# Optimization experiments

Measured on AMD Instinct MI355X. Metric: run time of the kernel, lower is better.

Reference implementation:

```python
import jax, jax.numpy as jnp
import numpy as np

D_IN = 300      # mol2vec feature dim
H = 64          # neurons[0] == neurons[1]


def _l2norm(x):
    # F.normalize(x, p=2, dim=-1)
    n = jnp.sqrt(jnp.sum(x * x, axis=-1, keepdims=True))
    return x / jnp.maximum(n, 1e-12)


def _scatter_mean(x, row, col, n_nodes):
    # scatter_mean(x[col], row, dim_size=n_nodes); empty rows -> 0
    s = jax.ops.segment_sum(x[col], row, num_segments=n_nodes)
    c = jax.ops.segment_sum(jnp.ones((row.shape[0], 1), x.dtype), row, num_segments=n_nodes)
    return s / jnp.maximum(c, 1.0)


def _sage_base(x, edges, W, b, n_nodes):
    agg = _scatter_mean(x, edges[0], edges[1], n_nodes)
    h = jnp.concatenate([agg, x], axis=1) @ W + b
    return _l2norm(h)


def _sage_deep(x1, x2, pos_e, neg_e, W, b, n_nodes):
    a1 = _scatter_mean(x1, pos_e[0], pos_e[1], n_nodes)
    a2 = _scatter_mean(x2, neg_e[0], neg_e[1], n_nodes)
    h = jnp.concatenate([a1, a2, x1], axis=1) @ W + b
    return _l2norm(h)


def setup_inputs() -> dict:
    key = jax.random.key(0)
    ks = jax.random.split(key, 16)
    N, E = 8192, 262144

    X = jax.random.normal(ks[0], (N, D_IN), dtype=jnp.float32)

    def make_edges(k):
        e = jax.random.randint(k, (2, E), 0, N, dtype=jnp.int64)
        # no self loops (module calls remove_self_loops)
        col = jnp.where(e[1] == e[0], (e[1] + 1) % N, e[1])
        return jnp.stack([e[0], col])

    positive_edges = make_edges(ks[1])
    negative_edges = make_edges(ks[2])

    labels = jax.random.normal(ks[3], (N * N,), dtype=jnp.float32)
    label_mask = jax.random.uniform(ks[4], (N, N), dtype=jnp.float32)

    sd = lambda fan_in: 1.0 / np.sqrt(fan_in)
    W_pos_base = jax.random.normal(ks[5], (2 * D_IN, H), dtype=jnp.float32) * sd(2 * D_IN)
    b_pos_base = jnp.zeros((H,), dtype=jnp.float32)
    W_neg_base = jax.random.normal(ks[6], (2 * D_IN, H), dtype=jnp.float32) * sd(2 * D_IN)
    b_neg_base = jnp.zeros((H,), dtype=jnp.float32)
    W_pos_deep = jax.random.normal(ks[7], (3 * H, H), dtype=jnp.float32) * sd(3 * H)
    b_pos_deep = jnp.zeros((H,), dtype=jnp.float32)
    W_neg_deep = jax.random.normal(ks[8], (3 * H, H), dtype=jnp.float32) * sd(3 * H)
    b_neg_deep = jnp.zeros((H,), dtype=jnp.float32)

    return {
        "X": X, "positive_edges": positive_edges, "negative_edges": negative_edges,
        "labels": labels, "label_mask": label_mask,
        "W_pos_base": W_pos_base, "b_pos_base": b_pos_base,
        "W_neg_base": W_neg_base, "b_neg_base": b_neg_base,
        "W_pos_deep": W_pos_deep, "b_pos_deep": b_pos_deep,
        "W_neg_deep": W_neg_deep, "b_neg_deep": b_neg_deep,
    }


def reference(X, positive_edges, negative_edges, labels, label_mask,
              W_pos_base, b_pos_base, W_neg_base, b_neg_base,
              W_pos_deep, b_pos_deep, W_neg_deep, b_neg_deep):
    N = X.shape[0]
    h_pos = jnp.tanh(_sage_base(X, positive_edges, W_pos_base, b_pos_base, N))
    h_neg = jnp.tanh(_sage_base(X, negative_edges, W_neg_base, b_neg_base, N))
    h_pos2 = jnp.tanh(_sage_deep(h_pos, h_neg, positive_edges, negative_edges, W_pos_deep, b_pos_deep, N))
    h_neg2 = jnp.tanh(_sage_deep(h_neg, h_pos, positive_edges, negative_edges, W_neg_deep, b_neg_deep, N))
    z = jnp.concatenate([h_pos2, h_neg2], axis=1)           # [N, 2H]
    X_mol = _l2norm(z)
    pred = ((X_mol @ X_mol.T) * label_mask).reshape(-1)      # [N*N]
    loss = jnp.mean((pred - labels) ** 2)
    return (loss, X_mol, pred)
```

## Files before the change

### kernel.cpp

```cpp
#include <hip/hip_runtime.h>
#include <hip/hip_bf16.h>

#define DIN 300
#define KP  320
#define NH  64

typedef __bf16 bf16x8 __attribute__((ext_vector_type(8)));
typedef float  f32x4  __attribute__((ext_vector_type(4)));

__device__ inline float wave_sum(float v){
#pragma unroll
  for (int m = 32; m >= 1; m >>= 1) v += __shfl_xor(v, m, 64);
  return v;
}

__global__ __launch_bounds__(256) void k_cvtX(const float* __restrict__ X,
                                              __hip_bfloat16* __restrict__ Xb){
  int row = blockIdx.x;
  const float* xr = X + (size_t)row * DIN;
  __hip_bfloat16* o = Xb + (size_t)row * KP;
  for (int k = threadIdx.x; k < KP; k += 256)
    o[k] = __float2bfloat16(k < DIN ? xr[k] : 0.f);
}

__global__ __launch_bounds__(256) void k_cvtW(const float* __restrict__ Wpb,
                                              const float* __restrict__ Wnb,
                                              __hip_bfloat16* __restrict__ Wtb){
  int c = blockIdx.x;
  int sel = c >> 6, jj = c & 63;
  const float* W = (sel < 2 ? Wpb : Wnb) + (size_t)(sel & 1) * DIN * NH + jj;
  __hip_bfloat16* o = Wtb + (size_t)c * KP;
  for (int k = threadIdx.x; k < KP; k += 256)
    o[k] = __float2bfloat16(k < DIN ? W[(size_t)k * NH] : 0.f);
}

__global__ __launch_bounds__(256) void k_gemm_base(const __hip_bfloat16* __restrict__ Xb,
                                                   const __hip_bfloat16* __restrict__ Wtb,
                                                   float* __restrict__ XW){
  const int wave = threadIdx.x >> 6, lane = threadIdx.x & 63;
  const int ti = blockIdx.y * 64 + wave * 16;
  const int cj = blockIdx.x * 64;
  const int r0 = lane & 15, kq = (lane >> 4) * 8;
  const unsigned short* Xp = (const unsigned short*)Xb;
  const unsigned short* Wp = (const unsigned short*)Wtb;
  f32x4 acc[4] = {};
  for (int ks = 0; ks < KP / 32; ++ks){
    int kb = ks * 32 + kq;
    bf16x8 a = *(const bf16x8*)(Xp + (size_t)(ti + r0) * KP + kb);
#pragma unroll
    for (int js = 0; js < 4; ++js){
      bf16x8 b = *(const bf16x8*)(Wp + (size_t)(cj + js * 16 + r0) * KP + kb);
      acc[js] = __builtin_amdgcn_mfma_f32_16x16x32_bf16(a, b, acc[js], 0, 0, 0);
    }
  }
  const int orow = ti + (lane >> 4) * 4;
  const int oc = cj + (lane & 15);
#pragma unroll
  for (int js = 0; js < 4; ++js)
#pragma unroll
    for (int i = 0; i < 4; ++i)
      XW[(size_t)(orow + i) * 256 + oc + js * 16] = acc[js][i];
}

__global__ void k_hist(const int* __restrict__ pr, const int* __restrict__ nr,
                       int* __restrict__ cp, int* __restrict__ cn, int E){
  int i = blockIdx.x * 256 + threadIdx.x;
  if (i < E){ atomicAdd(cp + pr[i], 1); atomicAdd(cn + nr[i], 1); }
}

__global__ __launch_bounds__(1024) void k_scan(const int* __restrict__ c0, int* __restrict__ o0,
                                               const int* __restrict__ c1, int* __restrict__ o1, int n){
  const int* cnt = blockIdx.x ? c1 : c0;
  int* off = blockIdx.x ? o1 : o0;
  __shared__ int lds[1024];
  int t = threadIdx.x;
  int ept = n >> 10;
  int s = 0;
  for (int i = 0; i < ept; ++i) s += cnt[t * ept + i];
  lds[t] = s; __syncthreads();
  for (int d = 1; d < 1024; d <<= 1){
    int add = (t >= d) ? lds[t - d] : 0;
    __syncthreads();
    lds[t] += add;
    __syncthreads();
  }
  int base = t ? lds[t - 1] : 0;
  for (int i = 0; i < ept; ++i){ off[t * ept + i] = base; base += cnt[t * ept + i]; }
}

__global__ void k_fill(const int* __restrict__ pr, const int* __restrict__ pc,
                       const int* __restrict__ nr, const int* __restrict__ nc,
                       const int* __restrict__ op, const int* __restrict__ on,
                       int* __restrict__ curp, int* __restrict__ curn,
                       int* __restrict__ adjp, int* __restrict__ adjn, int E){
  int i = blockIdx.x * 256 + threadIdx.x;
  if (i < E){
    int r = pr[i]; int p = atomicAdd(curp + r, 1); adjp[op[r] + p] = pc[i];
    r = nr[i];     p = atomicAdd(curn + r, 1);     adjn[on[r] + p] = nc[i];
  }
}

__device__ inline float gather_mean(const float* __restrict__ XW, const int* __restrict__ adj,
                                    int base, int d, int col){
  float s = 0.f; int j = 0;
  for (; j + 4 <= d; j += 4){
    int n0 = adj[base + j], n1 = adj[base + j + 1], n2 = adj[base + j + 2], n3 = adj[base + j + 3];
    s += XW[(size_t)n0 * 256 + col] + XW[(size_t)n1 * 256 + col]
       + XW[(size_t)n2 * 256 + col] + XW[(size_t)n3 * 256 + col];
  }
  for (; j < d; ++j) s += XW[(size_t)adj[base + j] * 256 + col];
  return s / (float)(d > 0 ? d : 1);
}

__global__ __launch_bounds__(256) void k_base(const float* __restrict__ XW,
    const int* __restrict__ adjp, const int* __restrict__ offp, const int* __restrict__ cntp,
    const int* __restrict__ adjn, const int* __restrict__ offn, const int* __restrict__ cntn,
    const float* __restrict__ bp, const float* __restrict__ bn,
    float* __restrict__ hp, float* __restrict__ hn){
  const int wave = threadIdx.x >> 6, lane = threadIdx.x & 63;
  const int node = blockIdx.x * 4 + wave;
  {
    float s = gather_mean(XW, adjp, offp[node], cntp[node], lane);
    float pre = s + XW[(size_t)node * 256 + 64 + lane] + bp[lane];
    float nrm = sqrtf(wave_sum(pre * pre));
    hp[(size_t)node * 64 + lane] = tanhf(pre / fmaxf(nrm, 1e-12f));
  }
  {
    float s = gather_mean(XW, adjn, offn[node], cntn[node], lane + 128);
    float pre = s + XW[(size_t)node * 256 + 192 + lane] + bn[lane];
    float nrm = sqrtf(wave_sum(pre * pre));
    hn[(size_t)node * 64 + lane] = tanhf(pre / fmaxf(nrm, 1e-12f));
  }
}

__global__ __launch_bounds__(256) void k_deep(const float* __restrict__ hp, const float* __restrict__ hn,
    const int* __restrict__ adjp, const int* __restrict__ offp, const int* __restrict__ cntp,
    const int* __restrict__ adjn, const int* __restrict__ offn, const int* __restrict__ cntn,
    const float* __restrict__ Wpd, const float* __restrict__ bpd,
    const float* __restrict__ Wnd, const float* __restrict__ bnd,
    float* __restrict__ xmol, __hip_bfloat16* __restrict__ Xmb){
  const int wave = threadIdx.x >> 6, lane = threadIdx.x & 63;
  const int node = blockIdx.x * 4 + wave;
  const float mhp = hp[(size_t)node * 64 + lane];
  const float mhn = hn[(size_t)node * 64 + lane];
  float a1p = 0.f, a1n = 0.f;
  {
    int d = cntp[node], base = offp[node]; int j = 0;
    for (; j + 2 <= d; j += 2){
      int n0 = adjp[base + j], n1 = adjp[base + j + 1];
      a1p += hp[(size_t)n0 * 64 + lane] + hp[(size_t)n1 * 64 + lane];
      a1n += hn[(size_t)n0 * 64 + lane] + hn[(size_t)n1 * 64 + lane];
    }
    for (; j < d; ++j){ int n0 = adjp[base + j]; a1p += hp[(size_t)n0 * 64 + lane]; a1n += hn[(size_t)n0 * 64 + lane]; }
    float inv = 1.f / (float)(d > 0 ? d : 1); a1p *= inv; a1n *= inv;
  }
  float a2p = 0.f, a2n = 0.f;
  {
    int d = cntn[node], base = offn[node]; int j = 0;
    for (; j + 2 <= d; j += 2){
      int n0 = adjn[base + j], n1 = adjn[base + j + 1];
      a2p += hn[(size_t)n0 * 64 + lane] + hn[(size_t)n1 * 64 + lane];
      a2n += hp[(size_t)n0 * 64 + lane] + hp[(size_t)n1 * 64 + lane];
    }
    for (; j < d; ++j){ int n0 = adjn[base + j]; a2p += hn[(size_t)n0 * 64 + lane]; a2n += hp[(size_t)n0 * 64 + lane]; }
    float inv = 1.f / (float)(d > 0 ? d : 1); a2p *= inv; a2n *= inv;
  }
  float accp = bpd[lane], accn = bnd[lane];
#pragma unroll 4
  for (int k = 0; k < 64; ++k){
    float p1 = __shfl(a1p, k, 64), p2 = __shfl(a2p, k, 64), p3 = __shfl(mhp, k, 64);
    float q1 = __shfl(a1n, k, 64), q2 = __shfl(a2n, k, 64), q3 = __shfl(mhn, k, 64);
    accp += p1 * Wpd[k * 64 + lane] + p2 * Wpd[(64 + k) * 64 + lane] + p3 * Wpd[(128 + k) * 64 + lane];
    accn += q1 * Wnd[k * 64 + lane] + q2 * Wnd[(64 + k) * 64 + lane] + q3 * Wnd[(128 + k) * 64 + lane];
  }
  float np = sqrtf(wave_sum(accp * accp));
  float h2p = tanhf(accp / fmaxf(np, 1e-12f));
  float nn = sqrtf(wave_sum(accn * accn));
  float h2n = tanhf(accn / fmaxf(nn, 1e-12f));
  float nz = sqrtf(wave_sum(h2p * h2p + h2n * h2n));
  float xp = h2p / fmaxf(nz, 1e-12f);
  float xn = h2n / fmaxf(nz, 1e-12f);
  xmol[(size_t)node * 128 + lane] = xp;
  xmol[(size_t)node * 128 + 64 + lane] = xn;
  Xmb[(size_t)node * 128 + lane] = __float2bfloat16(xp);
  Xmb[(size_t)node * 128 + 64 + lane] = __float2bfloat16(xn);
}

__global__ __launch_bounds__(256) void k_pred(const __hip_bfloat16* __restrict__ Xmb,
    const float* __restrict__ mask, const float* __restrict__ labels,
    float* __restrict__ pred, float* __restrict__ partial, int N){
  const int wave = threadIdx.x >> 6, lane = threadIdx.x & 63;
  const int ti = blockIdx.y * 64 + wave * 16;
  const int tj = blockIdx.x * 128;
  const int r0 = lane & 15, kq = (lane >> 4) * 8;
  const unsigned short* X = (const unsigned short*)Xmb;
  f32x4 acc[2][4] = {};
#pragma unroll
  for (int ks = 0; ks < 4; ++ks){
    int kb = ks * 32 + kq;
    bf16x8 a = *(const bf16x8*)(X + (size_t)(ti + r0) * 128 + kb);
#pragma unroll
    for (int pan = 0; pan < 2; ++pan)
#pragma unroll
      for (int js = 0; js < 4; ++js){
        bf16x8 b = *(const bf16x8*)(X + (size_t)(tj + pan * 64 + js * 16 + r0) * 128 + kb);
        acc[pan][js] = __builtin_amdgcn_mfma_f32_16x16x32_bf16(a, b, acc[pan][js], 0, 0, 0);
      }
  }
  __shared__ float tile[4][16][132];
  __shared__ float wsum[4];
  const int rb = (lane >> 4) * 4, c16 = lane & 15;
#pragma unroll
  for (int pan = 0; pan < 2; ++pan)
#pragma unroll
    for (int js = 0; js < 4; ++js)
#pragma unroll
      for (int i = 0; i < 4; ++i)
        tile[wave][rb + i][pan * 64 + js * 16 + c16] = acc[pan][js][i];
  const int hi = lane >> 5, c = lane & 31;
  f32x4 m[8], lb[8];
#pragma unroll
  for (int g = 0; g < 8; ++g){
    size_t idx = (size_t)(ti + g * 2 + hi) * N + tj + c * 4;
    m[g]  = __builtin_nontemporal_load((const f32x4*)(mask + idx));
    lb[g] = __builtin_nontemporal_load((const f32x4*)(labels + idx));
  }
  float lsum = 0.f;
#pragma unroll
  for (int g = 0; g < 8; ++g){
    int row = g * 2 + hi;
    f32x4 a = *(const f32x4*)&tile[wave][row][c * 4];
    f32x4 pv = a * m[g];
    f32x4 d = pv - lb[g];
    lsum += d[0]*d[0] + d[1]*d[1] + d[2]*d[2] + d[3]*d[3];
    size_t idx = (size_t)(ti + row) * N + tj + c * 4;
    __builtin_nontemporal_store(pv[0], pred + idx);
    __builtin_nontemporal_store(pv[1], pred + idx + 1);
    __builtin_nontemporal_store(pv[2], pred + idx + 2);
    __builtin_nontemporal_store(pv[3], pred + idx + 3);
  }
  lsum = wave_sum(lsum);
  if (lane == 0) wsum[wave] = lsum;
  __syncthreads();
  if (threadIdx.x == 0)
    partial[blockIdx.y * gridDim.x + blockIdx.x] = wsum[0] + wsum[1] + wsum[2] + wsum[3];
}

__global__ __launch_bounds__(1024) void k_loss_fin(const float* __restrict__ partial,
                                                   float* __restrict__ out, float inv, int n){
  float s = 0.f;
  for (int i = threadIdx.x; i < n; i += 1024) s += partial[i];
  s = wave_sum(s);
  __shared__ float ws[16];
  if ((threadIdx.x & 63) == 0) ws[threadIdx.x >> 6] = s;
  __syncthreads();
  if (threadIdx.x == 0){
    float t = 0.f;
#pragma unroll
    for (int w = 0; w < 16; ++w) t += ws[w];
    out[0] = t * inv;
  }
}

extern "C" void kernel_launch(void* const* d_in, const int* in_sizes, int n_in,
                              void* d_out, int out_size, void* d_ws, size_t ws_size,
                              hipStream_t stream){
  const float* X      = (const float*)d_in[0];
  const int*   pe     = (const int*)d_in[1];
  const int*   ne     = (const int*)d_in[2];
  const float* labels = (const float*)d_in[3];
  const float* mask   = (const float*)d_in[4];
  const float* Wpb    = (const float*)d_in[5];
  const float* bpb    = (const float*)d_in[6];
  const float* Wnb    = (const float*)d_in[7];
  const float* bnb    = (const float*)d_in[8];
  const float* Wpd    = (const float*)d_in[9];
  const float* bpd    = (const float*)d_in[10];
  const float* Wnd    = (const float*)d_in[11];
  const float* bnd    = (const float*)d_in[12];
  const int N = in_sizes[0] / DIN;
  const int E = in_sizes[1] / 2;

  char* ws = (char*)d_ws;
  size_t off = 0;
  auto alloc = [&](size_t bytes){ void* p = ws + off; off = (off + bytes + 255) & ~(size_t)255; return p; };
  float* XW            = (float*)alloc((size_t)N * 256 * 4);
  float* hp            = (float*)alloc((size_t)N * 64 * 4);
  float* hn            = (float*)alloc((size_t)N * 64 * 4);
  __hip_bfloat16* Xmb  = (__hip_bfloat16*)alloc((size_t)N * 128 * 2);
  __hip_bfloat16* Xb   = (__hip_bfloat16*)alloc((size_t)N * KP * 2);
  __hip_bfloat16* Wtb  = (__hip_bfloat16*)alloc((size_t)256 * KP * 2);
  int* adjp            = (int*)alloc((size_t)E * 4);
  int* adjn            = (int*)alloc((size_t)E * 4);
  char* zbase = ws + off;
  int* cntp            = (int*)alloc((size_t)N * 4);
  int* cntn            = (int*)alloc((size_t)N * 4);
  int* curp            = (int*)alloc((size_t)N * 4);
  int* curn            = (int*)alloc((size_t)N * 4);
  size_t zbytes = (size_t)((ws + off) - zbase);
  int* offp            = (int*)alloc((size_t)N * 4);
  int* offn            = (int*)alloc((size_t)N * 4);
  float* partial       = (float*)alloc((size_t)(N / 64) * (N / 128) * 4);
  (void)ws_size; (void)n_in; (void)out_size;

  float* out_loss = (float*)d_out;
  float* out_xmol = out_loss + 1;
  float* out_pred = out_xmol + (size_t)N * 128;

  hipMemsetAsync(zbase, 0, zbytes, stream);
  k_cvtX<<<N, 256, 0, stream>>>(X, Xb);
  k_cvtW<<<256, 256, 0, stream>>>(Wpb, Wnb, Wtb);
  k_gemm_base<<<dim3(4, N / 64), 256, 0, stream>>>(Xb, Wtb, XW);
  k_hist<<<(E + 255) / 256, 256, 0, stream>>>(pe, ne, cntp, cntn, E);
  k_scan<<<2, 1024, 0, stream>>>(cntp, offp, cntn, offn, N);
  k_fill<<<(E + 255) / 256, 256, 0, stream>>>(pe, pe + E, ne, ne + E, offp, offn, curp, curn, adjp, adjn, E);
  k_base<<<N / 4, 256, 0, stream>>>(XW, adjp, offp, cntp, adjn, offn, cntn, bpb, bnb, hp, hn);
  k_deep<<<N / 4, 256, 0, stream>>>(hp, hn, adjp, offp, cntp, adjn, offn, cntn,
                                    Wpd, bpd, Wnd, bnd, out_xmol, Xmb);
  k_pred<<<dim3(N / 128, N / 64), 256, 0, stream>>>(Xmb, mask, labels, out_pred, partial, N);
  k_loss_fin<<<1, 1024, 0, stream>>>(partial, out_loss, 1.0f / ((float)N * (float)N), (N / 64) * (N / 128));
}
```

Before: 365.3 us.

## Make k_pred persistent over column chunks with double-buffered mask/label loads

Each k_pred block now walks a 2048-column chunk in 16 tiles of 128 columns instead of handling one tile. The A fragment stays in registers across tiles, and mask/label loads for the next tile are issued before the current tile is consumed, using two register buffers and sched barriers. This aims to overlap the memory-bound mask/label streaming with MFMA work and cut block launch overhead. The cost is higher register pressure (launch bounds now ask for 2 blocks per SIMD) and far fewer blocks, which may reduce latency hiding.

```diff
diff --git a/kernel.cpp b/kernel.cpp
--- a/kernel.cpp
+++ b/kernel.cpp
@@ -4,6 +4,8 @@
 #define DIN 300
 #define KP  320
 #define NH  64
+#define CHUNK 2048
+#define NT (CHUNK / 128)
 
 typedef __bf16 bf16x8 __attribute__((ext_vector_type(8)));
 typedef float  f32x4  __attribute__((ext_vector_type(4)));
@@ -186,59 +188,88 @@
   Xmb[(size_t)node * 128 + 64 + lane] = __float2bfloat16(xn);
 }
 
-__global__ __launch_bounds__(256) void k_pred(const __hip_bfloat16* __restrict__ Xmb,
+__global__ __launch_bounds__(256, 2) void k_pred(const __hip_bfloat16* __restrict__ Xmb,
     const float* __restrict__ mask, const float* __restrict__ labels,
     float* __restrict__ pred, float* __restrict__ partial, int N){
   const int wave = threadIdx.x >> 6, lane = threadIdx.x & 63;
   const int ti = blockIdx.y * 64 + wave * 16;
-  const int tj = blockIdx.x * 128;
+  const int cbase = blockIdx.x * CHUNK;
   const int r0 = lane & 15, kq = (lane >> 4) * 8;
   const unsigned short* X = (const unsigned short*)Xmb;
-  f32x4 acc[2][4] = {};
-#pragma unroll
-  for (int ks = 0; ks < 4; ++ks){
-    int kb = ks * 32 + kq;
-    bf16x8 a = *(const bf16x8*)(X + (size_t)(ti + r0) * 128 + kb);
-#pragma unroll
-    for (int pan = 0; pan < 2; ++pan)
-#pragma unroll
-      for (int js = 0; js < 4; ++js){
-        bf16x8 b = *(const bf16x8*)(X + (size_t)(tj + pan * 64 + js * 16 + r0) * 128 + kb);
-        acc[pan][js] = __builtin_amdgcn_mfma_f32_16x16x32_bf16(a, b, acc[pan][js], 0, 0, 0);
-      }
-  }
+
+  bf16x8 a[4];
+#pragma unroll
+  for (int ks = 0; ks < 4; ++ks)
+    a[ks] = *(const bf16x8*)(X + (size_t)(ti + r0) * 128 + ks * 32 + kq);
+
   __shared__ float tile[4][16][132];
   __shared__ float wsum[4];
+  const int hi = lane >> 5, c = lane & 31;
   const int rb = (lane >> 4) * 4, c16 = lane & 15;
-#pragma unroll
-  for (int pan = 0; pan < 2; ++pan)
-#pragma unroll
-    for (int js = 0; js < 4; ++js)
-#pragma unroll
-      for (int i = 0; i < 4; ++i)
-        tile[wave][rb + i][pan * 64 + js * 16 + c16] = acc[pan][js][i];
-  const int hi = lane >> 5, c = lane & 31;
-  f32x4 m[8], lb[8];
-#pragma unroll
-  for (int g = 0; g < 8; ++g){
-    size_t idx = (size_t)(ti + g * 2 + hi) * N + tj + c * 4;
-    m[g]  = __builtin_nontemporal_load((const f32x4*)(mask + idx));
-    lb[g] = __builtin_nontemporal_load((const f32x4*)(labels + idx));
-  }
+
   float lsum = 0.f;
-#pragma unroll
-  for (int g = 0; g < 8; ++g){
-    int row = g * 2 + hi;
-    f32x4 a = *(const f32x4*)&tile[wave][row][c * 4];
-    f32x4 pv = a * m[g];
-    f32x4 d = pv - lb[g];
-    lsum += d[0]*d[0] + d[1]*d[1] + d[2]*d[2] + d[3]*d[3];
-    size_t idx = (size_t)(ti + row) * N + tj + c * 4;
-    __builtin_nontemporal_store(pv[0], pred + idx);
-    __builtin_nontemporal_store(pv[1], pred + idx + 1);
-    __builtin_nontemporal_store(pv[2], pred + idx + 2);
-    __builtin_nontemporal_store(pv[3], pred + idx + 3);
-  }
+  f32x4 mA[8], lA[8], mB[8], lB[8];
+
+  auto ISSUE = [&](f32x4* mm, f32x4* ll, int t){
+    int tj = cbase + t * 128;
+#pragma unroll
+    for (int g = 0; g < 8; ++g){
+      size_t idx = (size_t)(ti + g * 2 + hi) * N + tj + c * 4;
+      mm[g] = __builtin_nontemporal_load((const f32x4*)(mask + idx));
+      ll[g] = __builtin_nontemporal_load((const f32x4*)(labels + idx));
+    }
+    __builtin_amdgcn_sched_barrier(0);
+  };
+  auto MFMA_T = [&](int t){
+    int tj = cbase + t * 128;
+    f32x4 acc[2][4] = {};
+#pragma unroll
+    for (int ks = 0; ks < 4; ++ks){
+      int kb = ks * 32 + kq;
+#pragma unroll
+      for (int pan = 0; pan < 2; ++pan)
+#pragma unroll
+        for (int js = 0; js < 4; ++js){
+          bf16x8 b = *(const bf16x8*)(X + (size_t)(tj + pan * 64 + js * 16 + r0) * 128 + kb);
+          acc[pan][js] = __builtin_amdgcn_mfma_f32_16x16x32_bf16(a[ks], b, acc[pan][js], 0, 0, 0);
+        }
+    }
+#pragma unroll
+    for (int pan = 0; pan < 2; ++pan)
+#pragma unroll
+      for (int js = 0; js < 4; ++js)
+#pragma unroll
+        for (int i = 0; i < 4; ++i)
+          tile[wave][rb + i][pan * 64 + js * 16 + c16] = acc[pan][js][i];
+  };
+  auto CONSUME = [&](const f32x4* mm, const f32x4* ll, int t){
+    int tj = cbase + t * 128;
+#pragma unroll
+    for (int g = 0; g < 8; ++g){
+      int row = g * 2 + hi;
+      f32x4 av = *(const f32x4*)&tile[wave][row][c * 4];
+      f32x4 pv = av * mm[g];
+      f32x4 d = pv - ll[g];
+      lsum += d[0]*d[0] + d[1]*d[1] + d[2]*d[2] + d[3]*d[3];
+      size_t idx = (size_t)(ti + row) * N + tj + c * 4;
+      __builtin_nontemporal_store(pv[0], pred + idx);
+      __builtin_nontemporal_store(pv[1], pred + idx + 1);
+      __builtin_nontemporal_store(pv[2], pred + idx + 2);
+      __builtin_nontemporal_store(pv[3], pred + idx + 3);
+    }
+  };
+
+  ISSUE(mA, lA, 0);
+#pragma unroll 1
+  for (int t = 0; t < NT; t += 2){
+    MFMA_T(t);
+    ISSUE(mB, lB, t + 1);
+    CONSUME(mA, lA, t);
+    MFMA_T(t + 1);
+    if (t + 2 < NT) ISSUE(mA, lA, t + 2);
+    CONSUME(mB, lB, t + 1);
+  }
+
   lsum = wave_sum(lsum);
   if (lane == 0) wsum[wave] = lsum;
   __syncthreads();
@@ -300,7 +331,7 @@
   size_t zbytes = (size_t)((ws + off) - zbase);
   int* offp            = (int*)alloc((size_t)N * 4);
   int* offn            = (int*)alloc((size_t)N * 4);
-  float* partial       = (float*)alloc((size_t)(N / 64) * (N / 128) * 4);
+  float* partial       = (float*)alloc((size_t)(N / 64) * (N / CHUNK) * 4);
   (void)ws_size; (void)n_in; (void)out_size;
 
   float* out_loss = (float*)d_out;
@@ -317,6 +348,6 @@
   k_base<<<N / 4, 256, 0, stream>>>(XW, adjp, offp, cntp, adjn, offn, cntn, bpb, bnb, hp, hn);
   k_deep<<<N / 4, 256, 0, stream>>>(hp, hn, adjp, offp, cntp, adjn, offn, cntn,
                                     Wpd, bpd, Wnd, bnd, out_xmol, Xmb);
-  k_pred<<<dim3(N / 128, N / 64), 256, 0, stream>>>(Xmb, mask, labels, out_pred, partial, N);
-  k_loss_fin<<<1, 1024, 0, stream>>>(partial, out_loss, 1.0f / ((float)N * (float)N), (N / 64) * (N / 128));
-}
+  k_pred<<<dim3(N / CHUNK, N / 64), 256, 0, stream>>>(Xmb, mask, labels, out_pred, partial, N);
+  k_loss_fin<<<1, 1024, 0, stream>>>(partial, out_loss, 1.0f / ((float)N * (float)N), (N / 64) * (N / CHUNK));
+}
```

Result: slower. 422.5 us (+15.6%).
